# Kernel tuning notes

Hardware: AMD Instinct MI355X
Metric: run time of the kernel (lower is better)

The kernel has to match this reference:

```python
import jax, jax.numpy as jnp
import numpy as np

N, M, NNZ, D = 50000, 20000, 400000, 256
ALPHA, BETA = 0.1, 0.5


def setup_inputs() -> dict:
    key = jax.random.key(0)
    ks = jax.random.split(key, 7)
    X = jax.random.normal(ks[0], (N, D), dtype=jnp.float32)
    X0 = jax.random.normal(ks[1], (N, D), dtype=jnp.float32)
    W = jax.random.normal(ks[2], (D, D), dtype=jnp.float32) / np.sqrt(D)
    degV = jax.random.uniform(ks[3], (N, 1), dtype=jnp.float32, minval=0.1, maxval=1.0)
    degE = jax.random.uniform(ks[4], (M, 1), dtype=jnp.float32, minval=0.1, maxval=1.0)
    vertex = jax.random.randint(ks[5], (NNZ,), 0, N, dtype=jnp.int32)
    edges = jax.random.randint(ks[6], (NNZ,), 0, M, dtype=jnp.int32)
    alpha = jnp.float32(ALPHA)
    beta = jnp.float32(BETA)
    return {"X": X, "X0": X0, "W": W, "degV": degV, "degE": degE,
            "vertex": vertex, "edges": edges, "alpha": alpha, "beta": beta}


def _normalize_l2(X):
    # torch: rownorm is detached -> treat scale as constant w.r.t. grad
    rownorm = jax.lax.stop_gradient(jnp.linalg.norm(X, axis=1, keepdims=True))
    scale = jnp.where(rownorm > 0, 1.0 / rownorm, 0.0)
    return X * scale


def reference(X, X0, W, degV, degE, vertex, edges, alpha, beta):
    # hop 1: gather node features to incidences, mean-aggregate into hyperedges
    Xve = X[vertex]                                               # [NNZ, D]
    sums = jax.ops.segment_sum(Xve, edges, num_segments=M)        # [M, D]
    cnts = jax.ops.segment_sum(jnp.ones((NNZ,), X.dtype), edges, num_segments=M)
    Xe = sums / jnp.maximum(cnts, 1.0)[:, None]                   # mean (first_aggregate)
    Xe = Xe * degE
    # hop 2: gather edge features back to incidences, sum-aggregate into nodes
    Xev = Xe[edges]                                               # [NNZ, D]
    Xv = jax.ops.segment_sum(Xev, vertex, num_segments=N)         # [N, D]
    Xv = Xv * degV
    Xn = _normalize_l2(Xv)                                        # use_norm=True
    Xi = (1.0 - alpha) * Xn + alpha * X0
    out = (1.0 - beta) * Xi + beta * (Xi @ W)
    return out
```

## Files before the change

### kernel.cpp

```cpp
#include <hip/hip_runtime.h>
#include <cstdint>

static constexpr int DD = 256;
static constexpr int SNB = 64;

typedef unsigned short ushort_t;
typedef __attribute__((ext_vector_type(8))) short short8v;
typedef __attribute__((ext_vector_type(4))) float f32x4;

static __device__ inline ushort_t f2bf(float f) {
  uint32_t u = __builtin_bit_cast(uint32_t, f);
  uint32_t r = (u + 0x7fffu + ((u >> 16) & 1u)) >> 16;
  return (ushort_t)r;
}
static __device__ inline float bf2f(ushort_t u) {
  return __builtin_bit_cast(float, (uint32_t)u << 16);
}
static __device__ inline void addbf8(float* a, int4 x) {
  uint32_t ux = (uint32_t)x.x, uy = (uint32_t)x.y;
  uint32_t uz = (uint32_t)x.z, uw = (uint32_t)x.w;
  a[0] += __builtin_bit_cast(float, ux << 16);
  a[1] += __builtin_bit_cast(float, ux & 0xFFFF0000u);
  a[2] += __builtin_bit_cast(float, uy << 16);
  a[3] += __builtin_bit_cast(float, uy & 0xFFFF0000u);
  a[4] += __builtin_bit_cast(float, uz << 16);
  a[5] += __builtin_bit_cast(float, uz & 0xFFFF0000u);
  a[6] += __builtin_bit_cast(float, uw << 16);
  a[7] += __builtin_bit_cast(float, uw & 0xFFFF0000u);
}


__global__ void k_count(const int* __restrict__ vertex, const int* __restrict__ edges,
                        int* __restrict__ cntV, int* __restrict__ cntE, int nnz) {
  int i = blockIdx.x * blockDim.x + threadIdx.x;
  if (i < nnz) {
    atomicAdd(&cntV[vertex[i]], 1);
    atomicAdd(&cntE[edges[i]], 1);
  }
}

__device__ inline int wave_incl_scan(int v, int lane) {
  #pragma unroll
  for (int o = 1; o < 64; o <<= 1) {
    int u = __shfl_up(v, o);
    if (lane >= o) v += u;
  }
  return v;
}

__global__ __launch_bounds__(256) void k_bsum(const int* __restrict__ cntE,
                                              const int* __restrict__ cntV,
                                              int* __restrict__ bsum, int M, int N) {
  int arr = blockIdx.x >> 6;
  int b = blockIdx.x & 63;
  const int* cnt = arr ? cntV : cntE;
  int n = arr ? N : M;
  int chunk = (((n + SNB - 1) / SNB) + 3) & ~3;
  int lo = b * chunk, hi = min(lo + chunk, n);
  int s = 0;
  for (int i = lo + (int)threadIdx.x; i < hi; i += 256) s += cnt[i];
  #pragma unroll
  for (int o = 32; o; o >>= 1) s += __shfl_down(s, o);
  __shared__ int sh[4];
  if ((threadIdx.x & 63) == 0) sh[threadIdx.x >> 6] = s;
  __syncthreads();
  if (threadIdx.x == 0) bsum[blockIdx.x] = sh[0] + sh[1] + sh[2] + sh[3];
}

__global__ __launch_bounds__(256) void k_woffs2(const int* __restrict__ cntE,
                                                const int* __restrict__ cntV,
                                                const int* __restrict__ bsum,
                                                int* __restrict__ offsE, int* __restrict__ curE,
                                                int* __restrict__ offsV, int* __restrict__ curV,
                                                int M, int N) {
  __shared__ int sbpre[128];
  int tid = threadIdx.x;
  if (tid < 128) {
    int v = bsum[tid];
    int inc = wave_incl_scan(v, tid & 63);
    sbpre[tid] = inc - v;
    if (blockIdx.x == 0 && (tid & 63) == 63) {
      if (tid < 64) offsE[M] = inc;
      else          offsV[N] = inc;
    }
  }
  __syncthreads();

  int arr = blockIdx.x >> 6;
  int b = blockIdx.x & 63;
  const int* cnt = arr ? cntV : cntE;
  int* offs = arr ? offsV : offsE;
  int* cur  = arr ? curV  : curE;
  int n = arr ? N : M;
  int chunk = (((n + SNB - 1) / SNB) + 3) & ~3;
  int lo = b * chunk, hi = min(lo + chunk, n);
  if (lo >= n) return;
  int base = sbpre[blockIdx.x];

  int idx = lo + (int)threadIdx.x * 4;
  int c0 = 0, c1 = 0, c2 = 0, c3 = 0;
  if (idx + 3 < hi) {
    int4 c = *reinterpret_cast<const int4*>(cnt + idx);
    c0 = c.x; c1 = c.y; c2 = c.z; c3 = c.w;
  } else if (idx < hi) {
    c0 = cnt[idx];
    if (idx + 1 < hi) c1 = cnt[idx + 1];
    if (idx + 2 < hi) c2 = cnt[idx + 2];
  }
  int tsum = c0 + c1 + c2 + c3;
  int lane = threadIdx.x & 63, wid = threadIdx.x >> 6;
  int winc = wave_incl_scan(tsum, lane);
  __shared__ int wtot[4];
  if (lane == 63) wtot[wid] = winc;
  __syncthreads();
  int wbase = 0;
  #pragma unroll
  for (int q = 0; q < 4; ++q) wbase += (q < wid) ? wtot[q] : 0;
  int excl = base + wbase + winc - tsum;
  int o0 = excl, o1 = o0 + c0, o2 = o1 + c1, o3 = o2 + c2;
  if (idx + 3 < hi) {
    *reinterpret_cast<int4*>(offs + idx) = make_int4(o0, o1, o2, o3);
    *reinterpret_cast<int4*>(cur + idx)  = make_int4(o0, o1, o2, o3);
  } else if (idx < hi) {
    offs[idx] = o0; cur[idx] = o0;
    if (idx + 1 < hi) { offs[idx + 1] = o1; cur[idx + 1] = o1; }
    if (idx + 2 < hi) { offs[idx + 2] = o2; cur[idx + 2] = o2; }
  }
}


__global__ void k_fillx(const int* __restrict__ vertex, const int* __restrict__ edges,
                        int* __restrict__ curE, int* __restrict__ curV,
                        ushort_t* __restrict__ incEv, ushort_t* __restrict__ incVe,
                        int nnz, int nb,
                        const float* __restrict__ X, ushort_t* __restrict__ Xbf,
                        int total4, int xb,
                        const float* __restrict__ W, const float* __restrict__ beta_p,
                        ushort_t* __restrict__ Wt) {
  int b = blockIdx.x;
  if (b < nb) {
    int i = b * 256 + (int)threadIdx.x;
    if (i < nnz) {
      int v = vertex[i], e = edges[i];
      int pe = atomicAdd(&curE[e], 1);
      incEv[pe] = (ushort_t)v;
      int pv = atomicAdd(&curV[v], 1);
      incVe[pv] = (ushort_t)e;
    }
  } else if (b < nb + xb) {
    int i = (b - nb) * 256 + (int)threadIdx.x;
    if (i < total4) {
      float4 v = reinterpret_cast<const float4*>(X)[i];
      ushort4 r;
      r.x = f2bf(v.x); r.y = f2bf(v.y); r.z = f2bf(v.z); r.w = f2bf(v.w);
      reinterpret_cast<ushort4*>(Xbf)[i] = r;
    }
  } else {
    int t = (b - nb - xb) * 256 + (int)threadIdx.x;
    int k = t >> 8, c = t & 255;
    float beta = beta_p[0];
    float val = beta * W[t] + ((k == c) ? (1.0f - beta) : 0.0f);
    Wt[c * 256 + k] = f2bf(val);
  }
}


__global__ void k_hop1(const ushort_t* __restrict__ Xbf, const float* __restrict__ degE,
                       const int* __restrict__ offsE, const ushort_t* __restrict__ incEv,
                       ushort_t* __restrict__ Xe, int M) {
  int gw = (blockIdx.x * blockDim.x + threadIdx.x) >> 6;
  int lane = threadIdx.x & 63;
  if (gw >= M) return;
  int half = lane >> 5, sub = lane & 31;
  int s = offsE[gw], t = offsE[gw + 1];
  float acc[8] = {0.f, 0.f, 0.f, 0.f, 0.f, 0.f, 0.f, 0.f};
  const ushort_t* rowbase = Xbf + sub * 8;
  int k = s;
  for (; k + 8 <= t; k += 8) {
    int4 x[4];
    #pragma unroll
    for (int p = 0; p < 4; ++p) {
      int lo = incEv[k + 2 * p], hi = incEv[k + 2 * p + 1];
      int v = half ? hi : lo;
      x[p] = *reinterpret_cast<const int4*>(rowbase + (size_t)v * DD);
    }
    #pragma unroll
    for (int p = 0; p < 4; ++p) addbf8(acc, x[p]);
  }
  for (; k < t; k += 2) {
    int idx = k + half;
    if (idx < t) {
      int v = incEv[idx];
      int4 x = *reinterpret_cast<const int4*>(rowbase + (size_t)v * DD);
      addbf8(acc, x);
    }
  }
  #pragma unroll
  for (int j = 0; j < 8; ++j) acc[j] += __shfl_xor(acc[j], 32);
  float scale = degE[gw] / fmaxf((float)(t - s), 1.0f);
  float b0 = half ? acc[4] : acc[0];
  float b1 = half ? acc[5] : acc[1];
  float b2 = half ? acc[6] : acc[2];
  float b3 = half ? acc[7] : acc[3];
  ushort4 r;
  r.x = f2bf(b0 * scale); r.y = f2bf(b1 * scale);
  r.z = f2bf(b2 * scale); r.w = f2bf(b3 * scale);
  *reinterpret_cast<ushort4*>(Xe + (size_t)gw * DD + sub * 8 + half * 4) = r;
}


__global__ void k_hop2(const ushort_t* __restrict__ Xe, const float* __restrict__ X0,
                       const float* __restrict__ degV, const int* __restrict__ offsV,
                       const ushort_t* __restrict__ incVe, const float* __restrict__ alpha_p,
                       float* __restrict__ Xi, int N) {
  int gw = (blockIdx.x * blockDim.x + threadIdx.x) >> 6;
  int lane = threadIdx.x & 63;
  if (gw >= N) return;
  int half = lane >> 5, sub = lane & 31;
  int s = offsV[gw], t = offsV[gw + 1];
  float acc[8] = {0.f, 0.f, 0.f, 0.f, 0.f, 0.f, 0.f, 0.f};
  const ushort_t* rowbase = Xe + sub * 8;
  int k = s;
  for (; k + 8 <= t; k += 8) {
    int4 x[4];
    #pragma unroll
    for (int p = 0; p < 4; ++p) {
      int lo = incVe[k + 2 * p], hi = incVe[k + 2 * p + 1];
      int e = half ? hi : lo;
      x[p] = *reinterpret_cast<const int4*>(rowbase + (size_t)e * DD);
    }
    #pragma unroll
    for (int p = 0; p < 4; ++p) addbf8(acc, x[p]);
  }
  for (; k < t; k += 2) {
    int idx = k + half;
    if (idx < t) {
      int e = incVe[idx];
      int4 x = *reinterpret_cast<const int4*>(rowbase + (size_t)e * DD);
      addbf8(acc, x);
    }
  }
  #pragma unroll
  for (int j = 0; j < 8; ++j) acc[j] += __shfl_xor(acc[j], 32);
  float dv = degV[gw];
  float b0 = (half ? acc[4] : acc[0]) * dv;
  float b1 = (half ? acc[5] : acc[1]) * dv;
  float b2 = (half ? acc[6] : acc[2]) * dv;
  float b3 = (half ? acc[7] : acc[3]) * dv;
  float ss = b0 * b0 + b1 * b1 + b2 * b2 + b3 * b3;
  #pragma unroll
  for (int o = 1; o < 64; o <<= 1) ss += __shfl_xor(ss, o);
  float norm = sqrtf(ss);
  float scl = (norm > 0.f) ? (1.0f / norm) : 0.f;
  float a = alpha_p[0];
  float oma = 1.0f - a;
  int f0 = sub * 8 + half * 4;
  float4 x0 = *reinterpret_cast<const float4*>(X0 + (size_t)gw * DD + f0);
  float4 r;
  r.x = oma * (b0 * scl) + a * x0.x;
  r.y = oma * (b1 * scl) + a * x0.y;
  r.z = oma * (b2 * scl) + a * x0.z;
  r.w = oma * (b3 * scl) + a * x0.w;
  *reinterpret_cast<float4*>(Xi + (size_t)gw * DD + f0) = r;
}


__global__ __launch_bounds__(512, 4) void k_gemm_mfma(float* XiOut,
                                                      const ushort_t* __restrict__ Wt,
                                                      int nrows) {
  __shared__ ushort_t A_lds[128][36];
  __shared__ ushort_t B_lds[256][36];
  const int tid = threadIdx.x;
  const int lane = tid & 63;
  const int wid = tid >> 6;
  const int wr = wid >> 2;
  const int wc = wid & 3;
  const int l15 = lane & 15;
  const int l4  = lane >> 4;
  const int row0 = blockIdx.x * 128;

  const int t2   = tid & 1;
  const int arow = tid >> 1;

  f32x4 acc[4][4];
  #pragma unroll
  for (int m = 0; m < 4; ++m)
    #pragma unroll
    for (int n = 0; n < 4; ++n) acc[m][n] = (f32x4){0.f, 0.f, 0.f, 0.f};

  for (int k0 = 0; k0 < 256; k0 += 32) {
    if (arow < 128) {
      int grow = row0 + arow;
      float4 v0 = make_float4(0.f, 0.f, 0.f, 0.f), v1 = v0, v2 = v0, v3 = v0;
      if (grow < nrows) {
        const float* src = XiOut + (size_t)grow * 256 + k0 + t2 * 16;
        v0 = *reinterpret_cast<const float4*>(src + 0);
        v1 = *reinterpret_cast<const float4*>(src + 4);
        v2 = *reinterpret_cast<const float4*>(src + 8);
        v3 = *reinterpret_cast<const float4*>(src + 12);
      }
      uint4 pk0, pk1;
      pk0.x = (uint32_t)f2bf(v0.x) | ((uint32_t)f2bf(v0.y) << 16);
      pk0.y = (uint32_t)f2bf(v0.z) | ((uint32_t)f2bf(v0.w) << 16);
      pk0.z = (uint32_t)f2bf(v1.x) | ((uint32_t)f2bf(v1.y) << 16);
      pk0.w = (uint32_t)f2bf(v1.z) | ((uint32_t)f2bf(v1.w) << 16);
      pk1.x = (uint32_t)f2bf(v2.x) | ((uint32_t)f2bf(v2.y) << 16);
      pk1.y = (uint32_t)f2bf(v2.z) | ((uint32_t)f2bf(v2.w) << 16);
      pk1.z = (uint32_t)f2bf(v3.x) | ((uint32_t)f2bf(v3.y) << 16);
      pk1.w = (uint32_t)f2bf(v3.z) | ((uint32_t)f2bf(v3.w) << 16);
      *reinterpret_cast<uint4*>(&A_lds[arow][t2 * 16 + 0]) = pk0;
      *reinterpret_cast<uint4*>(&A_lds[arow][t2 * 16 + 8]) = pk1;
    }
    {
      const ushort_t* src = Wt + (size_t)arow * 256 + k0 + t2 * 16;
      int4 w0 = *reinterpret_cast<const int4*>(src + 0);
      int4 w1 = *reinterpret_cast<const int4*>(src + 8);
      *reinterpret_cast<int4*>(&B_lds[arow][t2 * 16 + 0]) = w0;
      *reinterpret_cast<int4*>(&B_lds[arow][t2 * 16 + 8]) = w1;
    }
    __syncthreads();
    short8v a[4], b[4];
    #pragma unroll
    for (int m = 0; m < 4; ++m)
      a[m] = *reinterpret_cast<const short8v*>(&A_lds[wr * 64 + m * 16 + l15][l4 * 8]);
    #pragma unroll
    for (int n = 0; n < 4; ++n)
      b[n] = *reinterpret_cast<const short8v*>(&B_lds[wc * 64 + n * 16 + l15][l4 * 8]);
    #pragma unroll
    for (int m = 0; m < 4; ++m)
      #pragma unroll
      for (int n = 0; n < 4; ++n)
        acc[m][n] = __builtin_amdgcn_mfma_f32_16x16x32_bf16(a[m], b[n], acc[m][n], 0, 0, 0);
    __syncthreads();
  }

  int rb0 = row0 + wr * 64;
  int cb0 = wc * 64;
  #pragma unroll
  for (int m = 0; m < 4; ++m) {
    #pragma unroll
    for (int j = 0; j < 4; ++j) {
      int r = rb0 + m * 16 + l4 * 4 + j;
      if (r < nrows) {
        #pragma unroll
        for (int n = 0; n < 4; ++n) {
          size_t idx = (size_t)r * 256 + cb0 + n * 16 + l15;
          XiOut[idx] = acc[m][n][j];
        }
      }
    }
  }
}


extern "C" void kernel_launch(void* const* d_in, const int* in_sizes, int n_in,
                              void* d_out, int out_size, void* d_ws, size_t ws_size,
                              hipStream_t stream) {
  const float* X     = (const float*)d_in[0];
  const float* X0    = (const float*)d_in[1];
  const float* W     = (const float*)d_in[2];
  const float* degV  = (const float*)d_in[3];
  const float* degE  = (const float*)d_in[4];
  const int*   vertex= (const int*)d_in[5];
  const int*   edges = (const int*)d_in[6];
  const float* alpha = (const float*)d_in[7];
  const float* beta  = (const float*)d_in[8];

  const int N   = in_sizes[3];
  const int M   = in_sizes[4];
  const int NNZ = in_sizes[5];

  auto r4 = [](int x) { return (x + 3) & ~3; };
  const int Mr = r4(M), Nr = r4(N);

  int* w = (int*)d_ws;
  int* cntE  = w; w += Mr;
  int* cntV  = w; w += Nr;
  int* offsE = w; w += r4(M + 1);
  int* offsV = w; w += r4(N + 1);
  int* curE  = w; w += Mr;
  int* curV  = w; w += Nr;
  int* bsum  = w; w += 128;
  ushort_t* incEv16 = (ushort_t*)w; w += (NNZ + 1) / 2;
  ushort_t* incVe16 = (ushort_t*)w; w += (NNZ + 1) / 2;
  uintptr_t p = (uintptr_t)w;
  p = (p + 15) & ~(uintptr_t)15;
  ushort_t* Wt = (ushort_t*)p;
  p += (size_t)256 * 256 * sizeof(ushort_t);
  ushort_t* Xe = (ushort_t*)p;

  float*    Xi  = (float*)d_out;
  ushort_t* Xbf = (ushort_t*)d_out;

  hipMemsetAsync(cntE, 0, (size_t)(Mr + Nr) * sizeof(int), stream);

  int nb = (NNZ + 255) / 256;
  int total4 = N * (DD / 4);
  int xb = (total4 + 255) / 256;
  k_count <<<nb, 256, 0, stream>>>(vertex, edges, cntV, cntE, NNZ);
  k_bsum  <<<2 * SNB, 256, 0, stream>>>(cntE, cntV, bsum, M, N);
  k_woffs2<<<2 * SNB, 256, 0, stream>>>(cntE, cntV, bsum, offsE, curE, offsV, curV, M, N);
  k_fillx <<<nb + xb + 256, 256, 0, stream>>>(vertex, edges, curE, curV,
                                              incEv16, incVe16, NNZ, nb,
                                              X, Xbf, total4, xb,
                                              W, beta, Wt);

  k_hop1<<<(M + 3) / 4, 256, 0, stream>>>(Xbf, degE, offsE, incEv16, Xe, M);
  k_hop2<<<(N + 3) / 4, 256, 0, stream>>>(Xe, X0, degV, offsV, incVe16, alpha, Xi, N);
  k_gemm_mfma<<<(N + 127) / 128, 512, 0, stream>>>(Xi, Wt, N);
}
```

Baseline: 192.2 us.

## Fuse CSR count, block sums and offset scan into one cooperative kernel

Replaces the memset plus three separate launches (count, block-sum, offset scan) with a single cooperative kernel of 1024 blocks that uses grid-wide syncs between phases. The goal is to remove launch overhead and inter-kernel gaps in the small CSR-building prologue. In exchange it relies on grid.sync, which has its own cost, and most of the 1024 blocks sit idle during the scan phases. It also requires all 1024 blocks to be co-resident for the cooperative launch to succeed.

```diff
diff --git a/kernel.cpp b/kernel.cpp
--- a/kernel.cpp
+++ b/kernel.cpp
@@ -1,5 +1,8 @@
 #include <hip/hip_runtime.h>
+#include <hip/hip_cooperative_groups.h>
 #include <cstdint>
+
+namespace cg = cooperative_groups;
 
 static constexpr int DD = 256;
 static constexpr int SNB = 64;
@@ -29,16 +32,6 @@
   a[7] += __builtin_bit_cast(float, uw & 0xFFFF0000u);
 }
 
-
-__global__ void k_count(const int* __restrict__ vertex, const int* __restrict__ edges,
-                        int* __restrict__ cntV, int* __restrict__ cntE, int nnz) {
-  int i = blockIdx.x * blockDim.x + threadIdx.x;
-  if (i < nnz) {
-    atomicAdd(&cntV[vertex[i]], 1);
-    atomicAdd(&cntE[edges[i]], 1);
-  }
-}
-
 __device__ inline int wave_incl_scan(int v, int lane) {
   #pragma unroll
   for (int o = 1; o < 64; o <<= 1) {
@@ -48,83 +41,100 @@
   return v;
 }
 
-__global__ __launch_bounds__(256) void k_bsum(const int* __restrict__ cntE,
-                                              const int* __restrict__ cntV,
-                                              int* __restrict__ bsum, int M, int N) {
-  int arr = blockIdx.x >> 6;
-  int b = blockIdx.x & 63;
-  const int* cnt = arr ? cntV : cntE;
-  int n = arr ? N : M;
-  int chunk = (((n + SNB - 1) / SNB) + 3) & ~3;
-  int lo = b * chunk, hi = min(lo + chunk, n);
-  int s = 0;
-  for (int i = lo + (int)threadIdx.x; i < hi; i += 256) s += cnt[i];
-  #pragma unroll
-  for (int o = 32; o; o >>= 1) s += __shfl_down(s, o);
+
+__global__ __launch_bounds__(256) void k_csr(const int* __restrict__ vertex,
+                                             const int* __restrict__ edges,
+                                             int* __restrict__ cntE,
+                                             int* __restrict__ cntV,
+                                             int* __restrict__ bsum,
+                                             int* __restrict__ offsE, int* __restrict__ curE,
+                                             int* __restrict__ offsV, int* __restrict__ curV,
+                                             int M, int N, int NNZ, int zeroTot) {
+  cg::grid_group grid = cg::this_grid();
+  const int gt = blockIdx.x * blockDim.x + threadIdx.x;
+  const int gs = gridDim.x * blockDim.x;
+
+  for (int i = gt; i < zeroTot; i += gs) cntE[i] = 0;
+  grid.sync();
+
+  for (int i = gt; i < NNZ; i += gs) {
+    atomicAdd(&cntV[vertex[i]], 1);
+    atomicAdd(&cntE[edges[i]], 1);
+  }
+  grid.sync();
+
   __shared__ int sh[4];
-  if ((threadIdx.x & 63) == 0) sh[threadIdx.x >> 6] = s;
-  __syncthreads();
-  if (threadIdx.x == 0) bsum[blockIdx.x] = sh[0] + sh[1] + sh[2] + sh[3];
-}
-
-__global__ __launch_bounds__(256) void k_woffs2(const int* __restrict__ cntE,
-                                                const int* __restrict__ cntV,
-                                                const int* __restrict__ bsum,
-                                                int* __restrict__ offsE, int* __restrict__ curE,
-                                                int* __restrict__ offsV, int* __restrict__ curV,
-                                                int M, int N) {
-  __shared__ int sbpre[128];
-  int tid = threadIdx.x;
-  if (tid < 128) {
-    int v = bsum[tid];
-    int inc = wave_incl_scan(v, tid & 63);
-    sbpre[tid] = inc - v;
-    if (blockIdx.x == 0 && (tid & 63) == 63) {
-      if (tid < 64) offsE[M] = inc;
-      else          offsV[N] = inc;
-    }
-  }
-  __syncthreads();
-
-  int arr = blockIdx.x >> 6;
-  int b = blockIdx.x & 63;
-  const int* cnt = arr ? cntV : cntE;
-  int* offs = arr ? offsV : offsE;
-  int* cur  = arr ? curV  : curE;
-  int n = arr ? N : M;
-  int chunk = (((n + SNB - 1) / SNB) + 3) & ~3;
-  int lo = b * chunk, hi = min(lo + chunk, n);
-  if (lo >= n) return;
-  int base = sbpre[blockIdx.x];
-
-  int idx = lo + (int)threadIdx.x * 4;
-  int c0 = 0, c1 = 0, c2 = 0, c3 = 0;
-  if (idx + 3 < hi) {
-    int4 c = *reinterpret_cast<const int4*>(cnt + idx);
-    c0 = c.x; c1 = c.y; c2 = c.z; c3 = c.w;
-  } else if (idx < hi) {
-    c0 = cnt[idx];
-    if (idx + 1 < hi) c1 = cnt[idx + 1];
-    if (idx + 2 < hi) c2 = cnt[idx + 2];
-  }
-  int tsum = c0 + c1 + c2 + c3;
-  int lane = threadIdx.x & 63, wid = threadIdx.x >> 6;
-  int winc = wave_incl_scan(tsum, lane);
-  __shared__ int wtot[4];
-  if (lane == 63) wtot[wid] = winc;
-  __syncthreads();
-  int wbase = 0;
-  #pragma unroll
-  for (int q = 0; q < 4; ++q) wbase += (q < wid) ? wtot[q] : 0;
-  int excl = base + wbase + winc - tsum;
-  int o0 = excl, o1 = o0 + c0, o2 = o1 + c1, o3 = o2 + c2;
-  if (idx + 3 < hi) {
-    *reinterpret_cast<int4*>(offs + idx) = make_int4(o0, o1, o2, o3);
-    *reinterpret_cast<int4*>(cur + idx)  = make_int4(o0, o1, o2, o3);
-  } else if (idx < hi) {
-    offs[idx] = o0; cur[idx] = o0;
-    if (idx + 1 < hi) { offs[idx + 1] = o1; cur[idx + 1] = o1; }
-    if (idx + 2 < hi) { offs[idx + 2] = o2; cur[idx + 2] = o2; }
+  if (blockIdx.x < 128) {
+    int arr = blockIdx.x >> 6;
+    int b = blockIdx.x & 63;
+    const int* cnt = arr ? cntV : cntE;
+    int n = arr ? N : M;
+    int chunk = (((n + SNB - 1) / SNB) + 3) & ~3;
+    int lo = b * chunk, hi = min(lo + chunk, n);
+    int s = 0;
+    for (int i = lo + (int)threadIdx.x; i < hi; i += 256) s += cnt[i];
+    #pragma unroll
+    for (int o = 32; o; o >>= 1) s += __shfl_down(s, o);
+    if ((threadIdx.x & 63) == 0) sh[threadIdx.x >> 6] = s;
+    __syncthreads();
+    if (threadIdx.x == 0) bsum[blockIdx.x] = sh[0] + sh[1] + sh[2] + sh[3];
+  }
+  grid.sync();
+
+  if (blockIdx.x < 128) {
+    __shared__ int sbpre[128];
+    int tid = threadIdx.x;
+    if (tid < 128) {
+      int v = bsum[tid];
+      int inc = wave_incl_scan(v, tid & 63);
+      sbpre[tid] = inc - v;
+      if (blockIdx.x == 0 && (tid & 63) == 63) {
+        if (tid < 64) offsE[M] = inc;
+        else          offsV[N] = inc;
+      }
+    }
+    __syncthreads();
+
+    int arr = blockIdx.x >> 6;
+    int b = blockIdx.x & 63;
+    const int* cnt = arr ? cntV : cntE;
+    int* offs = arr ? offsV : offsE;
+    int* cur  = arr ? curV  : curE;
+    int n = arr ? N : M;
+    int chunk = (((n + SNB - 1) / SNB) + 3) & ~3;
+    int lo = b * chunk, hi = min(lo + chunk, n);
+    if (lo < n) {
+      int base = sbpre[blockIdx.x];
+      int idx = lo + (int)threadIdx.x * 4;
+      int c0 = 0, c1 = 0, c2 = 0, c3 = 0;
+      if (idx + 3 < hi) {
+        int4 c = *reinterpret_cast<const int4*>(cnt + idx);
+        c0 = c.x; c1 = c.y; c2 = c.z; c3 = c.w;
+      } else if (idx < hi) {
+        c0 = cnt[idx];
+        if (idx + 1 < hi) c1 = cnt[idx + 1];
+        if (idx + 2 < hi) c2 = cnt[idx + 2];
+      }
+      int tsum = c0 + c1 + c2 + c3;
+      int lane = threadIdx.x & 63, wid = threadIdx.x >> 6;
+      int winc = wave_incl_scan(tsum, lane);
+      __shared__ int wtot[4];
+      if (lane == 63) wtot[wid] = winc;
+      __syncthreads();
+      int wbase = 0;
+      #pragma unroll
+      for (int q = 0; q < 4; ++q) wbase += (q < wid) ? wtot[q] : 0;
+      int excl = base + wbase + winc - tsum;
+      int o0 = excl, o1 = o0 + c0, o2 = o1 + c1, o3 = o2 + c2;
+      if (idx + 3 < hi) {
+        *reinterpret_cast<int4*>(offs + idx) = make_int4(o0, o1, o2, o3);
+        *reinterpret_cast<int4*>(cur + idx)  = make_int4(o0, o1, o2, o3);
+      } else if (idx < hi) {
+        offs[idx] = o0; cur[idx] = o0;
+        if (idx + 1 < hi) { offs[idx + 1] = o1; cur[idx + 1] = o1; }
+        if (idx + 2 < hi) { offs[idx + 2] = o2; cur[idx + 2] = o2; }
+      }
+    }
   }
 }
 
@@ -392,14 +402,18 @@
   float*    Xi  = (float*)d_out;
   ushort_t* Xbf = (ushort_t*)d_out;
 
-  hipMemsetAsync(cntE, 0, (size_t)(Mr + Nr) * sizeof(int), stream);
-
+  int zeroTot = Mr + Nr;
   int nb = (NNZ + 255) / 256;
   int total4 = N * (DD / 4);
   int xb = (total4 + 255) / 256;
-  k_count <<<nb, 256, 0, stream>>>(vertex, edges, cntV, cntE, NNZ);
-  k_bsum  <<<2 * SNB, 256, 0, stream>>>(cntE, cntV, bsum, M, N);
-  k_woffs2<<<2 * SNB, 256, 0, stream>>>(cntE, cntV, bsum, offsE, curE, offsV, curV, M, N);
+
+  {
+    void* args[] = {(void*)&vertex, (void*)&edges, (void*)&cntE, (void*)&cntV,
+                    (void*)&bsum, (void*)&offsE, (void*)&curE, (void*)&offsV,
+                    (void*)&curV, (void*)&M, (void*)&N, (void*)&NNZ, (void*)&zeroTot};
+    hipLaunchCooperativeKernel((void*)k_csr, dim3(1024), dim3(256), args, 0, stream);
+  }
+
   k_fillx <<<nb + xb + 256, 256, 0, stream>>>(vertex, edges, curE, curV,
                                               incEv16, incVe16, NNZ, nb,
                                               X, Xbf, total4, xb,
```

Result: slower. 462.6 us (+140.8%).
